# Optimization experiments

Measured on AMD Instinct MI355X. Metric: run time of the kernel, lower is better.

## Reference

```python
import jax, jax.numpy as jnp
import numpy as np


def setup_inputs() -> dict:
    key = jax.random.key(0)
    k1, k2 = jax.random.split(key)
    src = jax.random.normal(k1, (2, 1, 160, 192, 160), dtype=jnp.float32)
    flow = jax.random.normal(k2, (2, 3, 160, 192, 160), dtype=jnp.float32)
    return {"src": src, "flow": flow}


def _grid_sample_3d(src, z, y, x):
    """Trilinear grid_sample, padding_mode='zeros', align_corners=False semantics.

    src: [B, C, D, H, W]; z, y, x: absolute (unnormalized) sample coords [B, D, H, W].
    """
    B, C, D, H, W = src.shape
    z0 = jnp.floor(z); y0 = jnp.floor(y); x0 = jnp.floor(x)
    wz1 = z - z0; wy1 = y - y0; wx1 = x - x0
    wz0 = 1.0 - wz1; wy0 = 1.0 - wy1; wx0 = 1.0 - wx1

    def gather(zi, yi, xi):
        # zero padding: mask out-of-range taps, clamp indices for safe gather
        inb = ((zi >= 0) & (zi < D) & (yi >= 0) & (yi < H) & (xi >= 0) & (xi < W))
        zc = jnp.clip(zi, 0, D - 1).astype(jnp.int32)
        yc = jnp.clip(yi, 0, H - 1).astype(jnp.int32)
        xc = jnp.clip(xi, 0, W - 1).astype(jnp.int32)
        vals = jax.vmap(lambda s, a, b, c: s[:, a, b, c])(src, zc, yc, xc)  # [B,C,D,H,W]
        return vals * inb[:, None].astype(src.dtype)

    z1 = z0 + 1.0; y1 = y0 + 1.0; x1 = x0 + 1.0
    out = (
        gather(z0, y0, x0) * (wz0 * wy0 * wx0)[:, None]
        + gather(z0, y0, x1) * (wz0 * wy0 * wx1)[:, None]
        + gather(z0, y1, x0) * (wz0 * wy1 * wx0)[:, None]
        + gather(z0, y1, x1) * (wz0 * wy1 * wx1)[:, None]
        + gather(z1, y0, x0) * (wz1 * wy0 * wx0)[:, None]
        + gather(z1, y0, x1) * (wz1 * wy0 * wx1)[:, None]
        + gather(z1, y1, x0) * (wz1 * wy1 * wx0)[:, None]
        + gather(z1, y1, x1) * (wz1 * wy1 * wx1)[:, None]
    )
    return out


def reference(src, flow):
    B, C, D, H, W = src.shape
    dims = (D, H, W)
    # identity meshgrid (ij indexing) added to the flow field
    idz, idy, idx = jnp.meshgrid(
        jnp.arange(D, dtype=flow.dtype),
        jnp.arange(H, dtype=flow.dtype),
        jnp.arange(W, dtype=flow.dtype),
        indexing="ij",
    )
    new_locs = jnp.stack([idz, idy, idx])[None] + flow  # [B,3,D,H,W]
    # per-axis normalization to [-1,1]: 2*(p/(S-1) - 0.5)
    scale = jnp.array([2.0 / (s - 1) for s in dims], dtype=flow.dtype).reshape(1, 3, 1, 1, 1)
    g = new_locs * scale - 1.0  # same as 2*(p/(S-1)-0.5)
    gz, gy, gx = g[:, 0], g[:, 1], g[:, 2]
    # grid_sample unnormalization, align_corners=False: p = ((g+1)*S - 1)/2
    z = ((gz + 1.0) * D - 1.0) * 0.5
    y = ((gy + 1.0) * H - 1.0) * 0.5
    x = ((gx + 1.0) * W - 1.0) * 0.5
    return _grid_sample_3d(src, z, y, x)
```

## Files before the change

kernel.cpp:

```cpp
#include <hip/hip_runtime.h>

#define B_ 2
#define D_ 160
#define H_ 192
#define W_ 160

constexpr int HW_  = H_ * W_;
constexpr int DHW_ = D_ * HW_;

#define TX 32
#define TY 8
#define TZ 8
#define HLO 4
#define SXT 44
#define SYT 17
#define SZT 17
#define NSLOT (SZT * SYT * 11)

__global__ __launch_bounds__(256) void st3d_kernel(const float* __restrict__ src,
                                                   const float* __restrict__ flow,
                                                   float* __restrict__ out) {
    __shared__ float tile[SZT * SYT * SXT];

    const float SZ = (float)D_ / (float)(D_ - 1);
    const float SY = (float)H_ / (float)(H_ - 1);
    const float SX = (float)W_ / (float)(W_ - 1);

    const int bx  = blockIdx.x;
    const int by  = blockIdx.y;
    const int bzb = blockIdx.z;
    const int b   = bzb / (D_ / TZ);
    const int bz  = bzb % (D_ / TZ);

    const int oxi = bx * TX - HLO;
    const int oyi = by * TY - HLO;
    const int ozi = bz * TZ - HLO;

    const float* __restrict__ sp = src + (size_t)b * DHW_;
    const int tid = threadIdx.x;

    for (int l = tid; l < NSLOT; l += 256) {
        int x4  = l % 11;
        int rem = l / 11;
        int yy  = rem % SYT;
        int zz  = rem / SYT;
        int gz  = min(max(ozi + zz, 0), D_ - 1);
        int gy  = min(max(oyi + yy, 0), H_ - 1);
        int gx0 = oxi + x4 * 4;
        const float* rowp = sp + (size_t)gz * HW_ + (size_t)gy * W_;
        float4 v;
        if (gx0 >= 0 && gx0 <= W_ - 4) {
            v = *(const float4*)(rowp + gx0);
        } else {
            v.x = rowp[min(max(gx0 + 0, 0), W_ - 1)];
            v.y = rowp[min(max(gx0 + 1, 0), W_ - 1)];
            v.z = rowp[min(max(gx0 + 2, 0), W_ - 1)];
            v.w = rowp[min(max(gx0 + 3, 0), W_ - 1)];
        }
        *(float4*)&tile[(zz * SYT + yy) * SXT + x4 * 4] = v;
    }

    const int lxl = tid % TX;
    const int lyl = tid / TX;
    const int w = bx * TX + lxl;
    const int h = by * TY + lyl;
    const float* __restrict__ fb = flow + (size_t)b * 3 * DHW_;
    float fza[TZ], fya[TZ], fxa[TZ];
    #pragma unroll
    for (int k = 0; k < TZ; ++k) {
        int d = bz * TZ + k;
        int s = d * HW_ + h * W_ + w;
        fza[k] = fb[s];
        fya[k] = fb[DHW_ + s];
        fxa[k] = fb[2 * DHW_ + s];
    }

    __syncthreads();

    #pragma unroll
    for (int k = 0; k < TZ; ++k) {
        const int d = bz * TZ + k;
        const float z = (d + fza[k]) * SZ - 0.5f;
        const float y = (h + fya[k]) * SY - 0.5f;
        const float x = (w + fxa[k]) * SX - 0.5f;

        const float zf = floorf(z), yf = floorf(y), xf = floorf(x);
        const int z0 = (int)zf, y0 = (int)yf, x0 = (int)xf;
        const int z1 = z0 + 1, y1 = y0 + 1, x1 = x0 + 1;

        float wz1 = z - zf, wy1 = y - yf, wx1 = x - xf;
        float wz0 = 1.0f - wz1, wy0 = 1.0f - wy1, wx0 = 1.0f - wx1;

        wz0 = ((unsigned)z0 < (unsigned)D_) ? wz0 : 0.0f;
        wz1 = ((unsigned)z1 < (unsigned)D_) ? wz1 : 0.0f;
        wy0 = ((unsigned)y0 < (unsigned)H_) ? wy0 : 0.0f;
        wy1 = ((unsigned)y1 < (unsigned)H_) ? wy1 : 0.0f;
        wx0 = ((unsigned)x0 < (unsigned)W_) ? wx0 : 0.0f;
        wx1 = ((unsigned)x1 < (unsigned)W_) ? wx1 : 0.0f;

        const int z0c = min(max(z0, 0), D_ - 1), z1c = min(max(z1, 0), D_ - 1);
        const int y0c = min(max(y0, 0), H_ - 1), y1c = min(max(y1, 0), H_ - 1);
        const int x0c = min(max(x0, 0), W_ - 1), x1c = min(max(x1, 0), W_ - 1);

        float v000, v001, v010, v011, v100, v101, v110, v111;

        const bool inTile = ((unsigned)(z0c - ozi) <= SZT - 2) &&
                            ((unsigned)(y0c - oyi) <= SYT - 2) &&
                            ((unsigned)(x0c - oxi) <= SXT - 2);
        if (inTile) {
            const int az0 = z0c - ozi, az1 = z1c - ozi;
            const int ay0 = y0c - oyi, ay1 = y1c - oyi;
            const int ax0 = x0c - oxi, ax1 = x1c - oxi;
            const int r00 = (az0 * SYT + ay0) * SXT;
            const int r01 = (az0 * SYT + ay1) * SXT;
            const int r10 = (az1 * SYT + ay0) * SXT;
            const int r11 = (az1 * SYT + ay1) * SXT;
            v000 = tile[r00 + ax0]; v001 = tile[r00 + ax1];
            v010 = tile[r01 + ax0]; v011 = tile[r01 + ax1];
            v100 = tile[r10 + ax0]; v101 = tile[r10 + ax1];
            v110 = tile[r11 + ax0]; v111 = tile[r11 + ax1];
        } else {
            const float* p00 = sp + (size_t)z0c * HW_ + (size_t)y0c * W_;
            const float* p01 = sp + (size_t)z0c * HW_ + (size_t)y1c * W_;
            const float* p10 = sp + (size_t)z1c * HW_ + (size_t)y0c * W_;
            const float* p11 = sp + (size_t)z1c * HW_ + (size_t)y1c * W_;
            v000 = p00[x0c]; v001 = p00[x1c];
            v010 = p01[x0c]; v011 = p01[x1c];
            v100 = p10[x0c]; v101 = p10[x1c];
            v110 = p11[x0c]; v111 = p11[x1c];
        }

        const float r = ((v000 * wx0 + v001 * wx1) * wy0 + (v010 * wx0 + v011 * wx1) * wy1) * wz0
                      + ((v100 * wx0 + v101 * wx1) * wy0 + (v110 * wx0 + v111 * wx1) * wy1) * wz1;

        out[(size_t)b * DHW_ + (size_t)d * HW_ + (size_t)h * W_ + w] = r;
    }
}

extern "C" void kernel_launch(void* const* d_in, const int* in_sizes, int n_in,
                              void* d_out, int out_size, void* d_ws, size_t ws_size,
                              hipStream_t stream) {
    const float* src  = (const float*)d_in[0];
    const float* flow = (const float*)d_in[1];
    float* out = (float*)d_out;

    dim3 grid(W_ / TX, H_ / TY, (D_ / TZ) * B_);
    st3d_kernel<<<grid, dim3(256), 0, stream>>>(src, flow, out);
}
```

Baseline: 254.4 us.

## Split interior blocks: direct global-to-LDS tile loads and lerp-form sampling

Blocks whose halo tile lies fully inside the volume now fill shared memory with direct global-to-LDS 16-byte loads, skipping register staging and clamping. The border path batches all tile loads before the stores. Interior blocks sample with simplified in-tile indexing and a lerp-form trilinear blend with no bounds masking, and fall back to a global sampler otherwise. This aims to cut tile-fill latency and per-sample ALU work, at the cost of a larger code footprint and possible register pressure from the unrolled border path.

```diff
diff --git a/kernel.cpp b/kernel.cpp
--- a/kernel.cpp
+++ b/kernel.cpp
@@ -16,124 +16,214 @@
 #define SYT 17
 #define SZT 17
 #define NSLOT (SZT * SYT * 11)
+#define NITER 13
+#define TAILN (NSLOT - 256 * (NITER - 1))
+
+__device__ __forceinline__ void gload_lds16(const float* g, float* l) {
+    __builtin_amdgcn_global_load_lds(
+        (const __attribute__((address_space(1))) unsigned int*)g,
+        (__attribute__((address_space(3))) unsigned int*)l,
+        16, 0, 0);
+}
+
+__device__ __forceinline__ float sample_global(const float* __restrict__ sp,
+                                               float z, float y, float x) {
+    const float zf = floorf(z), yf = floorf(y), xf = floorf(x);
+    const int z0 = (int)zf, y0 = (int)yf, x0 = (int)xf;
+    const int z1 = z0 + 1, y1 = y0 + 1, x1 = x0 + 1;
+    float wz1 = z - zf, wy1 = y - yf, wx1 = x - xf;
+    float wz0 = 1.f - wz1, wy0 = 1.f - wy1, wx0 = 1.f - wx1;
+    wz0 = ((unsigned)z0 < (unsigned)D_) ? wz0 : 0.f;
+    wz1 = ((unsigned)z1 < (unsigned)D_) ? wz1 : 0.f;
+    wy0 = ((unsigned)y0 < (unsigned)H_) ? wy0 : 0.f;
+    wy1 = ((unsigned)y1 < (unsigned)H_) ? wy1 : 0.f;
+    wx0 = ((unsigned)x0 < (unsigned)W_) ? wx0 : 0.f;
+    wx1 = ((unsigned)x1 < (unsigned)W_) ? wx1 : 0.f;
+    const int z0c = min(max(z0, 0), D_ - 1), z1c = min(max(z1, 0), D_ - 1);
+    const int y0c = min(max(y0, 0), H_ - 1), y1c = min(max(y1, 0), H_ - 1);
+    const int x0c = min(max(x0, 0), W_ - 1), x1c = min(max(x1, 0), W_ - 1);
+    const float* p00 = sp + (size_t)z0c * HW_ + (size_t)y0c * W_;
+    const float* p01 = sp + (size_t)z0c * HW_ + (size_t)y1c * W_;
+    const float* p10 = sp + (size_t)z1c * HW_ + (size_t)y0c * W_;
+    const float* p11 = sp + (size_t)z1c * HW_ + (size_t)y1c * W_;
+    const float v000 = p00[x0c], v001 = p00[x1c];
+    const float v010 = p01[x0c], v011 = p01[x1c];
+    const float v100 = p10[x0c], v101 = p10[x1c];
+    const float v110 = p11[x0c], v111 = p11[x1c];
+    return ((v000 * wx0 + v001 * wx1) * wy0 + (v010 * wx0 + v011 * wx1) * wy1) * wz0
+         + ((v100 * wx0 + v101 * wx1) * wy0 + (v110 * wx0 + v111 * wx1) * wy1) * wz1;
+}
 
 __global__ __launch_bounds__(256) void st3d_kernel(const float* __restrict__ src,
                                                    const float* __restrict__ flow,
                                                    float* __restrict__ out) {
     __shared__ float tile[SZT * SYT * SXT];
 
-    const float SZ = (float)D_ / (float)(D_ - 1);
-    const float SY = (float)H_ / (float)(H_ - 1);
-    const float SX = (float)W_ / (float)(W_ - 1);
-
-    const int bx  = blockIdx.x;
-    const int by  = blockIdx.y;
-    const int bzb = blockIdx.z;
-    const int b   = bzb / (D_ / TZ);
-    const int bz  = bzb % (D_ / TZ);
+    const float SZf = (float)D_ / (float)(D_ - 1);
+    const float SYf = (float)H_ / (float)(H_ - 1);
+    const float SXf = (float)W_ / (float)(W_ - 1);
+
+    const int tid = threadIdx.x;
+    const int bx = blockIdx.x, by = blockIdx.y, bzb = blockIdx.z;
+    const int b  = bzb / (D_ / TZ);
+    const int bz = bzb % (D_ / TZ);
 
     const int oxi = bx * TX - HLO;
     const int oyi = by * TY - HLO;
     const int ozi = bz * TZ - HLO;
 
     const float* __restrict__ sp = src + (size_t)b * DHW_;
-    const int tid = threadIdx.x;
-
-    for (int l = tid; l < NSLOT; l += 256) {
-        int x4  = l % 11;
-        int rem = l / 11;
-        int yy  = rem % SYT;
-        int zz  = rem / SYT;
-        int gz  = min(max(ozi + zz, 0), D_ - 1);
-        int gy  = min(max(oyi + yy, 0), H_ - 1);
-        int gx0 = oxi + x4 * 4;
-        const float* rowp = sp + (size_t)gz * HW_ + (size_t)gy * W_;
-        float4 v;
-        if (gx0 >= 0 && gx0 <= W_ - 4) {
-            v = *(const float4*)(rowp + gx0);
-        } else {
-            v.x = rowp[min(max(gx0 + 0, 0), W_ - 1)];
-            v.y = rowp[min(max(gx0 + 1, 0), W_ - 1)];
-            v.z = rowp[min(max(gx0 + 2, 0), W_ - 1)];
-            v.w = rowp[min(max(gx0 + 3, 0), W_ - 1)];
-        }
-        *(float4*)&tile[(zz * SYT + yy) * SXT + x4 * 4] = v;
+    const bool interior = (bx >= 1) & (bx <= 3) & (by >= 1) & (by <= 22) & (bz >= 1) & (bz <= 18);
+
+    const int r0 = tid / 11;
+    int x4 = tid - r0 * 11;
+    int yy = r0 % 17;
+    int zz = r0 / 17;
+
+    if (interior) {
+        const float* gbase = sp + (size_t)ozi * HW_ + oyi * W_ + oxi;
+        #pragma unroll
+        for (int i = 0; i < NITER; ++i) {
+            if (i < NITER - 1 || tid < TAILN) {
+                gload_lds16(gbase + zz * HW_ + yy * W_ + 4 * x4,
+                            &tile[4 * (tid + 256 * i)]);
+            }
+            x4 += 3; if (x4 >= 11) { x4 -= 11; yy += 1; }
+            yy += 6; zz += 1; if (yy >= 17) { yy -= 17; zz += 1; }
+        }
+    } else {
+        float4 v[NITER];
+        int x4b = x4, yyb = yy, zzb = zz;
+        #pragma unroll
+        for (int i = 0; i < NITER; ++i) {
+            if (i < NITER - 1 || tid < TAILN) {
+                const int gz = min(max(ozi + zzb, 0), D_ - 1);
+                const int gy = min(max(oyi + yyb, 0), H_ - 1);
+                const int gx0 = oxi + 4 * x4b;
+                const float* rowp = sp + (size_t)gz * HW_ + (size_t)gy * W_;
+                if (gx0 >= 0 && gx0 <= W_ - 4) {
+                    v[i] = *(const float4*)(rowp + gx0);
+                } else {
+                    v[i].x = rowp[min(max(gx0 + 0, 0), W_ - 1)];
+                    v[i].y = rowp[min(max(gx0 + 1, 0), W_ - 1)];
+                    v[i].z = rowp[min(max(gx0 + 2, 0), W_ - 1)];
+                    v[i].w = rowp[min(max(gx0 + 3, 0), W_ - 1)];
+                }
+            }
+            x4b += 3; if (x4b >= 11) { x4b -= 11; yyb += 1; }
+            yyb += 6; zzb += 1; if (yyb >= 17) { yyb -= 17; zzb += 1; }
+        }
+        #pragma unroll
+        for (int i = 0; i < NITER; ++i) {
+            if (i < NITER - 1 || tid < TAILN)
+                *(float4*)&tile[4 * (tid + 256 * i)] = v[i];
+        }
     }
 
-    const int lxl = tid % TX;
-    const int lyl = tid / TX;
+    const int lxl = tid & (TX - 1);
+    const int lyl = tid >> 5;
     const int w = bx * TX + lxl;
     const int h = by * TY + lyl;
     const float* __restrict__ fb = flow + (size_t)b * 3 * DHW_;
+    const int s0 = (bz * TZ) * HW_ + h * W_ + w;
     float fza[TZ], fya[TZ], fxa[TZ];
     #pragma unroll
     for (int k = 0; k < TZ; ++k) {
-        int d = bz * TZ + k;
-        int s = d * HW_ + h * W_ + w;
-        fza[k] = fb[s];
-        fya[k] = fb[DHW_ + s];
-        fxa[k] = fb[2 * DHW_ + s];
+        fza[k] = fb[s0 + k * HW_];
+        fya[k] = fb[DHW_ + s0 + k * HW_];
+        fxa[k] = fb[2 * DHW_ + s0 + k * HW_];
     }
 
     __syncthreads();
 
-    #pragma unroll
-    for (int k = 0; k < TZ; ++k) {
-        const int d = bz * TZ + k;
-        const float z = (d + fza[k]) * SZ - 0.5f;
-        const float y = (h + fya[k]) * SY - 0.5f;
-        const float x = (w + fxa[k]) * SX - 0.5f;
-
-        const float zf = floorf(z), yf = floorf(y), xf = floorf(x);
-        const int z0 = (int)zf, y0 = (int)yf, x0 = (int)xf;
-        const int z1 = z0 + 1, y1 = y0 + 1, x1 = x0 + 1;
-
-        float wz1 = z - zf, wy1 = y - yf, wx1 = x - xf;
-        float wz0 = 1.0f - wz1, wy0 = 1.0f - wy1, wx0 = 1.0f - wx1;
-
-        wz0 = ((unsigned)z0 < (unsigned)D_) ? wz0 : 0.0f;
-        wz1 = ((unsigned)z1 < (unsigned)D_) ? wz1 : 0.0f;
-        wy0 = ((unsigned)y0 < (unsigned)H_) ? wy0 : 0.0f;
-        wy1 = ((unsigned)y1 < (unsigned)H_) ? wy1 : 0.0f;
-        wx0 = ((unsigned)x0 < (unsigned)W_) ? wx0 : 0.0f;
-        wx1 = ((unsigned)x1 < (unsigned)W_) ? wx1 : 0.0f;
-
-        const int z0c = min(max(z0, 0), D_ - 1), z1c = min(max(z1, 0), D_ - 1);
-        const int y0c = min(max(y0, 0), H_ - 1), y1c = min(max(y1, 0), H_ - 1);
-        const int x0c = min(max(x0, 0), W_ - 1), x1c = min(max(x1, 0), W_ - 1);
-
-        float v000, v001, v010, v011, v100, v101, v110, v111;
-
-        const bool inTile = ((unsigned)(z0c - ozi) <= SZT - 2) &&
-                            ((unsigned)(y0c - oyi) <= SYT - 2) &&
-                            ((unsigned)(x0c - oxi) <= SXT - 2);
-        if (inTile) {
-            const int az0 = z0c - ozi, az1 = z1c - ozi;
-            const int ay0 = y0c - oyi, ay1 = y1c - oyi;
-            const int ax0 = x0c - oxi, ax1 = x1c - oxi;
-            const int r00 = (az0 * SYT + ay0) * SXT;
-            const int r01 = (az0 * SYT + ay1) * SXT;
-            const int r10 = (az1 * SYT + ay0) * SXT;
-            const int r11 = (az1 * SYT + ay1) * SXT;
-            v000 = tile[r00 + ax0]; v001 = tile[r00 + ax1];
-            v010 = tile[r01 + ax0]; v011 = tile[r01 + ax1];
-            v100 = tile[r10 + ax0]; v101 = tile[r10 + ax1];
-            v110 = tile[r11 + ax0]; v111 = tile[r11 + ax1];
-        } else {
-            const float* p00 = sp + (size_t)z0c * HW_ + (size_t)y0c * W_;
-            const float* p01 = sp + (size_t)z0c * HW_ + (size_t)y1c * W_;
-            const float* p10 = sp + (size_t)z1c * HW_ + (size_t)y0c * W_;
-            const float* p11 = sp + (size_t)z1c * HW_ + (size_t)y1c * W_;
-            v000 = p00[x0c]; v001 = p00[x1c];
-            v010 = p01[x0c]; v011 = p01[x1c];
-            v100 = p10[x0c]; v101 = p10[x1c];
-            v110 = p11[x0c]; v111 = p11[x1c];
-        }
-
-        const float r = ((v000 * wx0 + v001 * wx1) * wy0 + (v010 * wx0 + v011 * wx1) * wy1) * wz0
-                      + ((v100 * wx0 + v101 * wx1) * wy0 + (v110 * wx0 + v111 * wx1) * wy1) * wz1;
-
-        out[(size_t)b * DHW_ + (size_t)d * HW_ + (size_t)h * W_ + w] = r;
+    const float c_y = h * SYf - 0.5f;
+    const float c_x = w * SXf - 0.5f;
+    const size_t obase = (size_t)b * DHW_ + (size_t)s0;
+
+    if (interior) {
+        #pragma unroll
+        for (int k = 0; k < TZ; ++k) {
+            const int d = bz * TZ + k;
+            const float z = fmaf(fza[k], SZf, d * SZf - 0.5f);
+            const float y = fmaf(fya[k], SYf, c_y);
+            const float x = fmaf(fxa[k], SXf, c_x);
+            const float zf = floorf(z), yf = floorf(y), xf = floorf(x);
+            const int az0 = (int)zf - ozi;
+            const int ay0 = (int)yf - oyi;
+            const int ax0 = (int)xf - oxi;
+            float r;
+            if (((unsigned)az0 <= SZT - 2) & ((unsigned)ay0 <= SYT - 2) & ((unsigned)ax0 <= SXT - 2)) {
+                const float tz = z - zf, ty = y - yf, tx = x - xf;
+                const int idx = (az0 * SYT + ay0) * SXT + ax0;
+                const float v000 = tile[idx],                 v001 = tile[idx + 1];
+                const float v010 = tile[idx + SXT],           v011 = tile[idx + SXT + 1];
+                const float v100 = tile[idx + SYT * SXT],     v101 = tile[idx + SYT * SXT + 1];
+                const float v110 = tile[idx + SYT * SXT + SXT], v111 = tile[idx + SYT * SXT + SXT + 1];
+                const float a0 = v000 + tx * (v001 - v000);
+                const float a1 = v010 + tx * (v011 - v010);
+                const float a2 = v100 + tx * (v101 - v100);
+                const float a3 = v110 + tx * (v111 - v110);
+                const float b0 = a0 + ty * (a1 - a0);
+                const float b1 = a2 + ty * (a3 - a2);
+                r = b0 + tz * (b1 - b0);
+            } else {
+                r = sample_global(sp, z, y, x);
+            }
+            out[obase + (size_t)k * HW_] = r;
+        }
+    } else {
+        #pragma unroll
+        for (int k = 0; k < TZ; ++k) {
+            const int d = bz * TZ + k;
+            const float z = fmaf(fza[k], SZf, d * SZf - 0.5f);
+            const float y = fmaf(fya[k], SYf, c_y);
+            const float x = fmaf(fxa[k], SXf, c_x);
+            const float zf = floorf(z), yf = floorf(y), xf = floorf(x);
+            const int z0 = (int)zf, y0 = (int)yf, x0 = (int)xf;
+            const int z1 = z0 + 1, y1 = y0 + 1, x1 = x0 + 1;
+            float wz1 = z - zf, wy1 = y - yf, wx1 = x - xf;
+            float wz0 = 1.f - wz1, wy0 = 1.f - wy1, wx0 = 1.f - wx1;
+            wz0 = ((unsigned)z0 < (unsigned)D_) ? wz0 : 0.f;
+            wz1 = ((unsigned)z1 < (unsigned)D_) ? wz1 : 0.f;
+            wy0 = ((unsigned)y0 < (unsigned)H_) ? wy0 : 0.f;
+            wy1 = ((unsigned)y1 < (unsigned)H_) ? wy1 : 0.f;
+            wx0 = ((unsigned)x0 < (unsigned)W_) ? wx0 : 0.f;
+            wx1 = ((unsigned)x1 < (unsigned)W_) ? wx1 : 0.f;
+            const int z0c = min(max(z0, 0), D_ - 1), z1c = min(max(z1, 0), D_ - 1);
+            const int y0c = min(max(y0, 0), H_ - 1), y1c = min(max(y1, 0), H_ - 1);
+            const int x0c = min(max(x0, 0), W_ - 1), x1c = min(max(x1, 0), W_ - 1);
+            float r;
+            const bool inTile = ((unsigned)(z0c - ozi) <= SZT - 2) &&
+                                ((unsigned)(y0c - oyi) <= SYT - 2) &&
+                                ((unsigned)(x0c - oxi) <= SXT - 2);
+            if (inTile) {
+                const int az0 = z0c - ozi, az1 = z1c - ozi;
+                const int ay0 = y0c - oyi, ay1 = y1c - oyi;
+                const int ax0 = x0c - oxi, ax1 = x1c - oxi;
+                const int q00 = (az0 * SYT + ay0) * SXT;
+                const int q01 = (az0 * SYT + ay1) * SXT;
+                const int q10 = (az1 * SYT + ay0) * SXT;
+                const int q11 = (az1 * SYT + ay1) * SXT;
+                const float v000 = tile[q00 + ax0], v001 = tile[q00 + ax1];
+                const float v010 = tile[q01 + ax0], v011 = tile[q01 + ax1];
+                const float v100 = tile[q10 + ax0], v101 = tile[q10 + ax1];
+                const float v110 = tile[q11 + ax0], v111 = tile[q11 + ax1];
+                r = ((v000 * wx0 + v001 * wx1) * wy0 + (v010 * wx0 + v011 * wx1) * wy1) * wz0
+                  + ((v100 * wx0 + v101 * wx1) * wy0 + (v110 * wx0 + v111 * wx1) * wy1) * wz1;
+            } else {
+                const float* p00 = sp + (size_t)z0c * HW_ + (size_t)y0c * W_;
+                const float* p01 = sp + (size_t)z0c * HW_ + (size_t)y1c * W_;
+                const float* p10 = sp + (size_t)z1c * HW_ + (size_t)y0c * W_;
+                const float* p11 = sp + (size_t)z1c * HW_ + (size_t)y1c * W_;
+                const float v000 = p00[x0c], v001 = p00[x1c];
+                const float v010 = p01[x0c], v011 = p01[x1c];
+                const float v100 = p10[x0c], v101 = p10[x1c];
+                const float v110 = p11[x0c], v111 = p11[x1c];
+                r = ((v000 * wx0 + v001 * wx1) * wy0 + (v010 * wx0 + v011 * wx1) * wy1) * wz0
+                  + ((v100 * wx0 + v101 * wx1) * wy0 + (v110 * wx0 + v111 * wx1) * wy1) * wz1;
+            }
+            out[obase + (size_t)k * HW_] = r;
+        }
     }
 }
 
```

After: 222.4 us. 12.6% less time.
